# Kernel tuning notes

Hardware: AMD Instinct MI355X
Metric: run time of the kernel (lower is better)

## Reference

```python
import jax, jax.numpy as jnp
import numpy as np

VOCAB = 32000
MAXLEN = 512
E = 768
H = 12
D = E // H  # 64
L = 6
F = int(E * 8 / 3)  # 2048
THETA = 10000.0
EPS = 1.1920929e-07  # torch.finfo(float32).eps, RMSNorm default


def _rms_norm(x, w):
    var = jnp.mean(x * x, axis=-1, keepdims=True)
    return x * jax.lax.rsqrt(var + EPS) * w


def _rope(x, cos, sin):
    # x: [B,H,C,D]; cos/sin: [C,D/2] (interleaved even/odd convention)
    xe = x[..., 0::2]
    xo = x[..., 1::2]
    re = xe * cos - xo * sin
    ro = xe * sin + xo * cos
    out = jnp.stack([re, ro], axis=-1)  # [B,H,C,D/2,2]
    return out.reshape(x.shape)


def setup_inputs() -> dict:
    key = jax.random.key(0)
    ks = jax.random.split(key, 13)
    s = 0.02
    ids = jax.random.randint(ks[0], (8, MAXLEN), 0, VOCAB)
    embed = jax.random.normal(ks[1], (VOCAB, E), jnp.float32) * s
    norm1_w = jnp.ones((L, E), jnp.float32)
    wq = jax.random.normal(ks[2], (L, E, H * D), jnp.float32) * s
    wk = jax.random.normal(ks[3], (L, E, H * D), jnp.float32) * s
    wv = jax.random.normal(ks[4], (L, E, H * D), jnp.float32) * s
    wo = jax.random.normal(ks[5], (L, H * D, E), jnp.float32) * s
    norm2_w = jnp.ones((L, E), jnp.float32)
    w_gate = jax.random.normal(ks[6], (L, E, F), jnp.float32) * s
    w_val = jax.random.normal(ks[7], (L, E, F), jnp.float32) * s
    w_out = jax.random.normal(ks[8], (L, F, E), jnp.float32) * s
    normf_w = jnp.ones((E,), jnp.float32)
    unembed = jax.random.normal(ks[9], (E, VOCAB), jnp.float32) * s
    return {"ids": ids, "embed": embed, "norm1_w": norm1_w, "wq": wq,
            "wk": wk, "wv": wv, "wo": wo, "norm2_w": norm2_w,
            "w_gate": w_gate, "w_val": w_val, "w_out": w_out,
            "normf_w": normf_w, "unembed": unembed}


def reference(ids, embed, norm1_w, wq, wk, wv, wo, norm2_w,
              w_gate, w_val, w_out, normf_w, unembed):
    B, C = ids.shape
    # RoPE caches [C, D/2]
    half_ids = jnp.arange(D // 2, dtype=jnp.float32)
    inv_freq = 1.0 / (THETA ** (2.0 * half_ids / D))
    angles = jnp.arange(C, dtype=jnp.float32)[:, None] * inv_freq[None, :]
    cos, sin = jnp.cos(angles), jnp.sin(angles)
    causal = jnp.tril(jnp.ones((C, C), bool))

    x = embed[ids]  # [B,C,E]
    for l in range(L):
        h = _rms_norm(x, norm1_w[l])
        q = (h @ wq[l]).reshape(B, C, H, D).transpose(0, 2, 1, 3)
        k = (h @ wk[l]).reshape(B, C, H, D).transpose(0, 2, 1, 3)
        v = (h @ wv[l]).reshape(B, C, H, D).transpose(0, 2, 1, 3)
        q = _rope(q, cos, sin)
        k = _rope(k, cos, sin)
        scores = jnp.einsum('bhqd,bhkd->bhqk', q, k) / jnp.sqrt(jnp.float32(D))
        scores = jnp.where(causal, scores, -jnp.inf)
        w = jax.nn.softmax(scores, axis=-1)
        attn = jnp.einsum('bhqk,bhkd->bhqd', w, v)
        attn = attn.transpose(0, 2, 1, 3).reshape(B, C, H * D)
        x = x + attn @ wo[l]
        h2 = _rms_norm(x, norm2_w[l])
        gated = jax.nn.silu(h2 @ w_gate[l]) * (h2 @ w_val[l])
        x = x + gated @ w_out[l]
    x = _rms_norm(x, normf_w)
    return x @ unembed  # [B,C,VOCAB]
```

## Files before the change

kernel.cpp:

```cpp
#include <hip/hip_runtime.h>
#include <hip/hip_bf16.h>
#include <stdint.h>

typedef __hip_bfloat16 bf16;
typedef unsigned short ushort_t;
typedef __attribute__((ext_vector_type(8))) short bf16x8;
typedef __attribute__((ext_vector_type(4))) float f32x4;

#define EPSV 1.1920929e-07f

__device__ __forceinline__ float bfu2f(uint32_t u) {
  union { uint32_t i; float f; } t; t.i = u << 16; return t.f;
}
__device__ __forceinline__ ushort_t f2bfu(float f) {
  bf16 h = __float2bfloat16(f);
  return *reinterpret_cast<ushort_t*>(&h);
}

#define BAR() __builtin_amdgcn_s_barrier()
#define SCHEDB() __builtin_amdgcn_sched_barrier(0)
#define WAIT_LGKM0() { asm volatile("s_waitcnt lgkmcnt(0)" ::: "memory"); SCHEDB(); }
#define WAIT_VM4() asm volatile("s_waitcnt vmcnt(4)" ::: "memory")
#define WAIT_VM0() asm volatile("s_waitcnt vmcnt(0)" ::: "memory")

__global__ void rope_table_kernel(float* __restrict__ cosT, float* __restrict__ sinT) {
  int i = blockIdx.x * 256 + threadIdx.x;
  if (i >= 512 * 32) return;
  int c = i >> 5, dp = i & 31;
  float inv = powf(10000.0f, -(2.0f * dp) / 64.0f);
  float a = (float)c * inv;
  cosT[i] = cosf(a);
  sinT[i] = sinf(a);
}

__global__ void embed_kernel(const int* __restrict__ ids, const float* __restrict__ emb,
                             float* __restrict__ x) {
  int t = blockIdx.x;
  int id = ids[t];
  const float4* s = (const float4*)(emb + (size_t)id * 768);
  float4* d = (float4*)(x + (size_t)t * 768);
  d[threadIdx.x] = s[threadIdx.x];
}

__global__ __launch_bounds__(256) void rmsnorm_kernel(const float* __restrict__ x,
                                                      const float* __restrict__ wgt,
                                                      bf16* __restrict__ out) {
  const int row = blockIdx.x;
  const int tid = threadIdx.x;
  const float* xr = x + (size_t)row * 768;
  float v0 = xr[tid], v1 = xr[tid + 256], v2 = xr[tid + 512];
  float s = v0 * v0 + v1 * v1 + v2 * v2;
#pragma unroll
  for (int d = 1; d < 64; d <<= 1) s += __shfl_xor(s, d);
  __shared__ float red[4];
  if ((tid & 63) == 0) red[tid >> 6] = s;
  __syncthreads();
  s = red[0] + red[1] + red[2] + red[3];
  float rs = rsqrtf(s * (1.0f / 768.0f) + EPSV);
  bf16* orow = out + (size_t)row * 768;
  orow[tid]       = __float2bfloat16(v0 * rs * wgt[tid]);
  orow[tid + 256] = __float2bfloat16(v1 * rs * wgt[tid + 256]);
  orow[tid + 512] = __float2bfloat16(v2 * rs * wgt[tid + 512]);
}

__global__ __launch_bounds__(256) void transpose_all_kernel(
    const float* __restrict__ wq, const float* __restrict__ wk,
    const float* __restrict__ wv, const float* __restrict__ wo,
    const float* __restrict__ wg, const float* __restrict__ wvl,
    const float* __restrict__ wout, const float* __restrict__ unemb,
    bf16* __restrict__ wqkvT, bf16* __restrict__ woT,
    bf16* __restrict__ wgvT, bf16* __restrict__ woutT,
    bf16* __restrict__ unembT) {
  int id = blockIdx.x;
  const float* src; bf16* dst; int K, N, tile;
  bool gvmode = false; int w2 = 0;
  if (id < 13824) {
    int m = id / 576; tile = id % 576;
    int l = m >> 2, w3 = m & 3;
    K = 768; N = 768;
    const float* s0 = (w3 == 0) ? wq : (w3 == 1) ? wk : (w3 == 2) ? wv : wo;
    src = s0 + (size_t)l * 768 * 768;
    dst = (w3 < 3) ? wqkvT + (size_t)l * 2304 * 768 + (size_t)w3 * 768 * 768
                   : woT + (size_t)l * 768 * 768;
  } else if (id < 32256) {
    int id2 = id - 13824; int m = id2 / 1536; tile = id2 % 1536;
    int l = m >> 1; w2 = m & 1;
    K = 768; N = 2048; gvmode = true;
    src = (w2 ? wvl : wg) + (size_t)l * 768 * 2048;
    dst = wgvT + (size_t)l * 4096 * 768;
  } else if (id < 41472) {
    int id2 = id - 32256; int l = id2 / 1536; tile = id2 % 1536;
    K = 2048; N = 768;
    src = wout + (size_t)l * 2048 * 768;
    dst = woutT + (size_t)l * 768 * 2048;
  } else {
    tile = id - 41472;
    K = 768; N = 32000;
    src = unemb; dst = unembT;
  }
  int ntn = N >> 5;
  int nt = (tile % ntn) << 5, kt = (tile / ntn) << 5;
  __shared__ float tl[32][33];
  int tx = threadIdx.x & 31, ty = threadIdx.x >> 5;
#pragma unroll
  for (int i = 0; i < 4; ++i)
    tl[ty + i * 8][tx] = src[(size_t)(kt + ty + i * 8) * N + nt + tx];
  __syncthreads();
#pragma unroll
  for (int i = 0; i < 4; ++i) {
    int n = nt + ty + i * 8;
    size_t nrow = gvmode ? (size_t)((n >> 7) * 256 + w2 * 128 + (n & 127)) : (size_t)n;
    dst[nrow * K + kt + tx] = __float2bfloat16(tl[tx][ty + i * 8]);
  }
}

template <int MODE>
__global__ __launch_bounds__(256) void gemm_bt(const bf16* __restrict__ A,
                                               const bf16* __restrict__ BT,
                                               void* __restrict__ C,
                                               int M, int N, int K) {
  __shared__ __align__(16) bf16 As[128 * 32];
  __shared__ __align__(16) bf16 Bs[128 * 32];
  const int tid = threadIdx.x;
  const int lane = tid & 63, w = tid >> 6;
  const int g = lane >> 4, lc = lane & 15;
  const int bm = blockIdx.y * 128, bn = blockIdx.x * 128;
  const int wm = (w >> 1) * 64, wn = (w & 1) * 64;

  f32x4 acc[4][4];
#pragma unroll
  for (int i = 0; i < 4; ++i)
#pragma unroll
    for (int j = 0; j < 4; ++j) acc[i][j] = (f32x4){0.f, 0.f, 0.f, 0.f};

  for (int k0 = 0; k0 < K; k0 += 32) {
    __syncthreads();
#pragma unroll
    for (int j = 0; j < 2; ++j) {
      int c = (w * 2 + j) * 64 + lane;
      int row = c >> 2, part = c & 3;
      const bf16* srcA = A + (size_t)(bm + row) * K + k0 + part * 8;
      const bf16* srcB = BT + (size_t)(bn + row) * K + k0 + part * 8;
      __builtin_amdgcn_global_load_lds((const __attribute__((address_space(1))) void*)srcA,
                                       (__attribute__((address_space(3))) void*)(As + (w * 2 + j) * 512),
                                       16, 0, 0);
      __builtin_amdgcn_global_load_lds((const __attribute__((address_space(1))) void*)srcB,
                                       (__attribute__((address_space(3))) void*)(Bs + (w * 2 + j) * 512),
                                       16, 0, 0);
    }
    __syncthreads();
    bf16x8 af[4], bfr[4];
#pragma unroll
    for (int mi = 0; mi < 4; ++mi)
      af[mi] = *(const bf16x8*)(As + (wm + mi * 16 + lc) * 32 + g * 8);
#pragma unroll
    for (int ni = 0; ni < 4; ++ni)
      bfr[ni] = *(const bf16x8*)(Bs + (wn + ni * 16 + lc) * 32 + g * 8);
#pragma unroll
    for (int mi = 0; mi < 4; ++mi)
#pragma unroll
      for (int ni = 0; ni < 4; ++ni)
        acc[mi][ni] = __builtin_amdgcn_mfma_f32_16x16x32_bf16(af[mi], bfr[ni], acc[mi][ni], 0, 0, 0);
  }

#pragma unroll
  for (int mi = 0; mi < 4; ++mi)
#pragma unroll
    for (int ni = 0; ni < 4; ++ni)
#pragma unroll
      for (int r = 0; r < 4; ++r) {
        size_t row = (size_t)bm + wm + mi * 16 + g * 4 + r;
        size_t col = (size_t)bn + wn + ni * 16 + lc;
        float v = acc[mi][ni][r];
        if (MODE == 0)      ((bf16*)C)[row * N + col] = __float2bfloat16(v);
        else if (MODE == 1) ((float*)C)[row * N + col] = v;
        else                ((float*)C)[row * N + col] += v;
      }
}

template <int MODE>
__global__ __launch_bounds__(512, 2) void gemm256(const bf16* __restrict__ A,
                                                  const bf16* __restrict__ BT,
                                                  void* __restrict__ C,
                                                  int M, int N, int K,
                                                  const float* __restrict__ cosT,
                                                  const float* __restrict__ sinT) {
  __shared__ __align__(16) bf16 lds[2][4][256 * 32];

  const int tid = threadIdx.x;
  const int lane = tid & 63, w = tid >> 6;
  const int wr = w >> 2, wc = w & 3;
  const int g = lane >> 4, lc = lane & 15;

  const int nwg = gridDim.x;
  const int q = nwg >> 3;
  const int wg = ((int)blockIdx.x & 7) * q + ((int)blockIdx.x >> 3);
  const int nby = M >> 8;
  const int bx = wg / nby, by = wg % nby;
  const int bm = by << 8, bn = bx << 8;

  const bf16* Ap = A + (size_t)bm * K;
  const bf16* Bp = BT + (size_t)bn * K;

  const int soff = (lc * 64) + ((((lane >> 4) ^ ((lane >> 1) & 3)) << 4));

  auto stage_half = [&](int buf, int slab, const bf16* Base, int kcol) {
#pragma unroll
    for (int j = 0; j < 2; ++j) {
      int half_id = w * 2 + j;
      int row = half_id * 16 + (lane >> 2);
      int s_log = (lane & 3) ^ ((lane >> 3) & 3);
      const bf16* src = Base + (size_t)row * K + kcol + s_log * 8;
      bf16* dst = &lds[buf][slab][half_id * 512];
      __builtin_amdgcn_global_load_lds((const __attribute__((address_space(1))) void*)src,
                                       (__attribute__((address_space(3))) void*)dst,
                                       16, 0, 0);
    }
  };

  f32x4 acc[8][4];
#pragma unroll
  for (int i = 0; i < 8; ++i)
#pragma unroll
    for (int j = 0; j < 4; ++j) acc[i][j] = (f32x4){0.f, 0.f, 0.f, 0.f};

  const int NT = K >> 6;

  stage_half(0, 0, Ap, 0);
  stage_half(0, 1, Bp, 0);
  stage_half(0, 2, Ap, 32);
  stage_half(0, 3, Bp, 32);

  bf16x8 aF[4], bF[4];

  auto ds_A = [&](int buf, int kk, int mh) {
#pragma unroll
    for (int i = 0; i < 4; ++i) {
      int byte = (wr * 128 + mh * 64 + i * 16) * 64 + soff;
      aF[i] = *(const bf16x8*)((const char*)&lds[buf][kk * 2][0] + byte);
    }
  };
  auto ds_B = [&](int buf, int kk) {
#pragma unroll
    for (int nf = 0; nf < 4; ++nf) {
      int rb = (MODE == 3) ? ((nf < 2) ? (wc * 32 + nf * 16) : (128 + wc * 32 + (nf - 2) * 16))
                           : (wc * 64 + nf * 16);
      int byte = rb * 64 + soff;
      bF[nf] = *(const bf16x8*)((const char*)&lds[buf][kk * 2 + 1][0] + byte);
    }
  };
  auto mfma16 = [&](int mh) {
    __builtin_amdgcn_s_setprio(1);
#pragma unroll
    for (int i = 0; i < 4; ++i)
#pragma unroll
      for (int nf = 0; nf < 4; ++nf)
        acc[mh * 4 + i][nf] =
            __builtin_amdgcn_mfma_f32_16x16x32_bf16(aF[i], bF[nf], acc[mh * 4 + i][nf], 0, 0, 0);
    __builtin_amdgcn_s_setprio(0);
  };

  for (int t = 0; t < NT; ++t) {
    const int buf = t & 1;
    const bool pf = (t + 1) < NT;
    const int knext = (t + 1) << 6;

    WAIT_VM4();
    BAR(); SCHEDB();
    if (pf) stage_half(buf ^ 1, 0, Ap, knext);
    ds_A(buf, 0, 0);
    ds_B(buf, 0);
    BAR();
    WAIT_LGKM0();
    mfma16(0);

    if (pf) stage_half(buf ^ 1, 1, Bp, knext);
    ds_A(buf, 0, 1);
    BAR();
    WAIT_LGKM0();
    mfma16(1);

    if (pf) { WAIT_VM4(); } else { WAIT_VM0(); }
    BAR(); SCHEDB();
    if (pf) stage_half(buf ^ 1, 2, Ap, knext + 32);
    ds_A(buf, 1, 0);
    ds_B(buf, 1);
    BAR();
    WAIT_LGKM0();
    mfma16(0);

    if (pf) stage_half(buf ^ 1, 3, Bp, knext + 32);
    ds_A(buf, 1, 1);
    BAR();
    WAIT_LGKM0();
    mfma16(1);
  }

  if (MODE == 3) {
    bf16* act = (bf16*)C;
#pragma unroll
    for (int mf = 0; mf < 8; ++mf)
#pragma unroll
      for (int nf = 0; nf < 2; ++nf)
#pragma unroll
        for (int r = 0; r < 4; ++r) {
          size_t row = (size_t)bm + wr * 128 + mf * 16 + g * 4 + r;
          size_t col = (size_t)(bn >> 1) + wc * 32 + nf * 16 + lc;
          float gg = acc[mf][nf][r];
          float vv = acc[mf][nf + 2][r];
          float sg = gg / (1.0f + __expf(-gg));
          act[row * 2048 + col] = __float2bfloat16(sg * vv);
        }
  } else if (MODE == 4) {
#pragma unroll
    for (int mf = 0; mf < 8; ++mf)
#pragma unroll
      for (int nf = 0; nf < 4; ++nf)
#pragma unroll
        for (int r = 0; r < 4; ++r) {
          int row = bm + wr * 128 + mf * 16 + g * 4 + r;
          int col = bn + wc * 64 + nf * 16 + lc;
          float v = acc[mf][nf][r];
          float p = __shfl_xor(v, 1);
          float outv = v;
          if (col < 1536) {
            int cpos = row & 511;
            int dp = (col & 63) >> 1;
            float cs = cosT[cpos * 32 + dp], sn = sinT[cpos * 32 + dp];
            float o = (col & 1) ? (p * sn + v * cs) : (v * cs - p * sn);
            outv = (col < 768) ? o * 0.125f : o;
          }
          ((bf16*)C)[(size_t)row * N + col] = __float2bfloat16(outv);
        }
  } else {
#pragma unroll
    for (int mf = 0; mf < 8; ++mf)
#pragma unroll
      for (int nf = 0; nf < 4; ++nf)
#pragma unroll
        for (int r = 0; r < 4; ++r) {
          size_t row = (size_t)bm + wr * 128 + mf * 16 + g * 4 + r;
          size_t col = (size_t)bn + wc * 64 + nf * 16 + lc;
          float v = acc[mf][nf][r];
          if (MODE == 0) ((bf16*)C)[row * N + col] = __float2bfloat16(v);
          else           ((float*)C)[row * N + col] = v;
        }
  }
}

__global__ __launch_bounds__(256) void attn_kernel(const bf16* __restrict__ qkv,
                                                   bf16* __restrict__ out) {
  const int qt = blockIdx.x;
  const int h  = blockIdx.y;
  const int b  = blockIdx.z;
  const int tid = threadIdx.x;
  const int lane = tid & 63, w = tid >> 6;
  const int g = lane >> 4, lc = lane & 15;

  __shared__ __align__(16) bf16 Ks[64 * 64];
  __shared__ __align__(16) bf16 Vt[64][72];
  __shared__ __align__(16) bf16 Pl[4][32][72];

  bf16x8 qa[2][2];
#pragma unroll
  for (int mi = 0; mi < 2; ++mi)
#pragma unroll
    for (int ks = 0; ks < 2; ++ks) {
      size_t t = (size_t)b * 512 + qt * 128 + w * 32 + mi * 16 + lc;
      qa[mi][ks] = *(const bf16x8*)(qkv + t * 2304 + h * 64 + ks * 32 + g * 8);
    }

  float m_r[2][4], l_r[2][4];
  f32x4 acc_o[2][4];
#pragma unroll
  for (int mi = 0; mi < 2; ++mi)
#pragma unroll
    for (int r = 0; r < 4; ++r) { m_r[mi][r] = -1e30f; l_r[mi][r] = 0.f; }
#pragma unroll
  for (int mi = 0; mi < 2; ++mi)
#pragma unroll
    for (int ni = 0; ni < 4; ++ni) acc_o[mi][ni] = (f32x4){0.f, 0.f, 0.f, 0.f};

  const int nkt = 2 * qt + 2;
  for (int kt = 0; kt < nkt; ++kt) {
    __syncthreads();
#pragma unroll
    for (int j = 0; j < 2; ++j) {
      int c = j * 256 + tid;
      int r = c >> 3;
      int s_log = (c & 7) ^ (r & 7);
      const bf16* src = qkv + ((size_t)b * 512 + kt * 64 + r) * 2304 + 768 + h * 64 + s_log * 8;
      bf16* dst = Ks + (j * 2048 + w * 512);
      __builtin_amdgcn_global_load_lds((const __attribute__((address_space(1))) void*)src,
                                       (__attribute__((address_space(3))) void*)dst,
                                       16, 0, 0);
    }
#pragma unroll
    for (int j = 0; j < 2; ++j) {
      int u = j * 256 + tid;
      int r = u >> 3, d0 = (u & 7) * 8;
      bf16x8 vv = *(const bf16x8*)(qkv + ((size_t)b * 512 + kt * 64 + r) * 2304 + 1536 + h * 64 + d0);
#pragma unroll
      for (int e = 0; e < 8; ++e)
        *(ushort_t*)&Vt[d0 + e][r] = (ushort_t)vv[e];
    }
    __syncthreads();

    f32x4 sacc[2][4];
#pragma unroll
    for (int mi = 0; mi < 2; ++mi)
#pragma unroll
      for (int ni = 0; ni < 4; ++ni) sacc[mi][ni] = (f32x4){0.f, 0.f, 0.f, 0.f};
#pragma unroll
    for (int ni = 0; ni < 4; ++ni) {
      int kr = ni * 16 + lc;
      const char* kb = (const char*)Ks + kr * 128;
      bf16x8 kb0 = *(const bf16x8*)(kb + ((g) ^ (kr & 7)) * 16);
      bf16x8 kb1 = *(const bf16x8*)(kb + ((4 + g) ^ (kr & 7)) * 16);
#pragma unroll
      for (int mi = 0; mi < 2; ++mi) {
        sacc[mi][ni] = __builtin_amdgcn_mfma_f32_16x16x32_bf16(qa[mi][0], kb0, sacc[mi][ni], 0, 0, 0);
        sacc[mi][ni] = __builtin_amdgcn_mfma_f32_16x16x32_bf16(qa[mi][1], kb1, sacc[mi][ni], 0, 0, 0);
      }
    }
    if (kt >= 2 * qt) {
#pragma unroll
      for (int mi = 0; mi < 2; ++mi)
#pragma unroll
        for (int ni = 0; ni < 4; ++ni)
#pragma unroll
          for (int r = 0; r < 4; ++r) {
            int ql = w * 32 + mi * 16 + g * 4 + r;
            int kl = ni * 16 + lc;
            if (kt * 64 + kl > qt * 128 + ql) sacc[mi][ni][r] = -1e30f;
          }
    }
#pragma unroll
    for (int mi = 0; mi < 2; ++mi) {
      float mx[4], sm[4], mn[4], sc[4];
#pragma unroll
      for (int r = 0; r < 4; ++r)
        mx[r] = fmaxf(fmaxf(sacc[mi][0][r], sacc[mi][1][r]), fmaxf(sacc[mi][2][r], sacc[mi][3][r]));
#pragma unroll
      for (int d = 1; d < 16; d <<= 1)
#pragma unroll
        for (int r = 0; r < 4; ++r) mx[r] = fmaxf(mx[r], __shfl_xor(mx[r], d));
#pragma unroll
      for (int r = 0; r < 4; ++r) {
        mn[r] = fmaxf(m_r[mi][r], mx[r]);
        sc[r] = __expf(m_r[mi][r] - mn[r]);
        sm[r] = 0.f;
      }
#pragma unroll
      for (int ni = 0; ni < 4; ++ni)
#pragma unroll
        for (int r = 0; r < 4; ++r) {
          float p = __expf(sacc[mi][ni][r] - mn[r]);
          sacc[mi][ni][r] = p;
          sm[r] += p;
        }
#pragma unroll
      for (int d = 1; d < 16; d <<= 1)
#pragma unroll
        for (int r = 0; r < 4; ++r) sm[r] += __shfl_xor(sm[r], d);
#pragma unroll
      for (int r = 0; r < 4; ++r) {
        l_r[mi][r] = l_r[mi][r] * sc[r] + sm[r];
        m_r[mi][r] = mn[r];
      }
#pragma unroll
      for (int ni = 0; ni < 4; ++ni)
#pragma unroll
        for (int r = 0; r < 4; ++r) acc_o[mi][ni][r] *= sc[r];
#pragma unroll
      for (int ni = 0; ni < 4; ++ni)
#pragma unroll
        for (int r = 0; r < 4; ++r)
          *(ushort_t*)&Pl[w][mi * 16 + g * 4 + r][ni * 16 + lc] = f2bfu(sacc[mi][ni][r]);
    }
    WAIT_LGKM0();
#pragma unroll
    for (int ks = 0; ks < 2; ++ks) {
      bf16x8 pa[2];
#pragma unroll
      for (int mi = 0; mi < 2; ++mi)
        pa[mi] = *(const bf16x8*)&Pl[w][mi * 16 + lc][ks * 32 + g * 8];
#pragma unroll
      for (int ni = 0; ni < 4; ++ni) {
        bf16x8 vb = *(const bf16x8*)&Vt[ni * 16 + lc][ks * 32 + g * 8];
#pragma unroll
        for (int mi = 0; mi < 2; ++mi)
          acc_o[mi][ni] = __builtin_amdgcn_mfma_f32_16x16x32_bf16(pa[mi], vb, acc_o[mi][ni], 0, 0, 0);
      }
    }
  }
#pragma unroll
  for (int mi = 0; mi < 2; ++mi) {
    float inv[4];
#pragma unroll
    for (int r = 0; r < 4; ++r) inv[r] = 1.0f / l_r[mi][r];
#pragma unroll
    for (int ni = 0; ni < 4; ++ni)
#pragma unroll
      for (int r = 0; r < 4; ++r) {
        size_t t = (size_t)b * 512 + qt * 128 + w * 32 + mi * 16 + g * 4 + r;
        int d = ni * 16 + lc;
        out[t * 768 + h * 64 + d] = __float2bfloat16(acc_o[mi][ni][r] * inv[r]);
      }
  }
}

extern "C" void kernel_launch(void* const* d_in, const int* in_sizes, int n_in,
                              void* d_out, int out_size, void* d_ws, size_t ws_size,
                              hipStream_t stream) {
  const int*   ids    = (const int*)d_in[0];
  const float* embedW = (const float*)d_in[1];
  const float* norm1w = (const float*)d_in[2];
  const float* wq     = (const float*)d_in[3];
  const float* wk     = (const float*)d_in[4];
  const float* wv     = (const float*)d_in[5];
  const float* wo     = (const float*)d_in[6];
  const float* norm2w = (const float*)d_in[7];
  const float* wgate  = (const float*)d_in[8];
  const float* wval   = (const float*)d_in[9];
  const float* wout   = (const float*)d_in[10];
  const float* normfw = (const float*)d_in[11];
  const float* unemb  = (const float*)d_in[12];

  char* arena = (char*)d_out;
  size_t off = 0;
  auto alloc = [&](size_t bytes) -> char* {
    char* p = arena + off;
    off += (bytes + 255) & ~(size_t)255;
    return p;
  };
  float* x       = (float*)alloc(4096ull * 768 * 4);
  bf16*  h       = (bf16*)alloc(4096ull * 768 * 2);
  bf16*  qkv     = (bf16*)alloc(4096ull * 2304 * 2);
  bf16*  attnout = (bf16*)alloc(4096ull * 768 * 2);
  bf16*  act     = (bf16*)alloc(4096ull * 2048 * 2);
  float* cosT    = (float*)alloc(512 * 32 * 4);
  float* sinT    = (float*)alloc(512 * 32 * 4);
  bf16*  wqkvT   = (bf16*)alloc(6ull * 2304 * 768 * 2);
  bf16*  woT     = (bf16*)alloc(6ull * 768 * 768 * 2);
  bf16*  wgvT    = (bf16*)alloc(6ull * 4096 * 768 * 2);
  bf16*  woutT   = (bf16*)alloc(6ull * 768 * 2048 * 2);

  bf16* unembT = (bf16*)d_ws;
  bf16* hf     = (bf16*)((char*)d_ws + 32000ull * 768 * 2);

  rope_table_kernel<<<64, 256, 0, stream>>>(cosT, sinT);
  embed_kernel<<<4096, 192, 0, stream>>>(ids, embedW, x);
  transpose_all_kernel<<<65472, 256, 0, stream>>>(wq, wk, wv, wo, wgate, wval, wout, unemb,
                                                  wqkvT, woT, wgvT, woutT, unembT);

  for (int l = 0; l < 6; ++l) {
    rmsnorm_kernel<<<4096, 256, 0, stream>>>(x, norm1w + (size_t)l * 768, h);
    gemm256<4><<<16 * 9, 512, 0, stream>>>(h, wqkvT + (size_t)l * 2304 * 768, qkv,
                                           4096, 2304, 768, cosT, sinT);
    attn_kernel<<<dim3(4, 12, 8), 256, 0, stream>>>(qkv, attnout);
    gemm_bt<2><<<dim3(6, 32), 256, 0, stream>>>(attnout, woT + (size_t)l * 768 * 768, x, 4096, 768, 768);
    rmsnorm_kernel<<<4096, 256, 0, stream>>>(x, norm2w + (size_t)l * 768, h);
    gemm256<3><<<16 * 16, 512, 0, stream>>>(h, wgvT + (size_t)l * 4096 * 768, act,
                                            4096, 4096, 768, nullptr, nullptr);
    gemm_bt<2><<<dim3(6, 32), 256, 0, stream>>>(act, woutT + (size_t)l * 768 * 2048, x, 4096, 768, 2048);
  }

  rmsnorm_kernel<<<4096, 256, 0, stream>>>(x, normfw, hf);
  gemm256<1><<<16 * 125, 512, 0, stream>>>(hf, unembT, (float*)d_out, 4096, 32000, 768,
                                           nullptr, nullptr);
}
```

Before: 1.736 ms.

## Split-K the projection GEMMs and fuse residual reduction with RMSNorm

The wo and w_out GEMMs, which previously launched only 192 blocks and did read-modify-write on x, now use split-K (2 and 4 slices) and write partial sums to a new fp32 buffer. A new reduce kernel adds the partials to the residual and computes the next RMSNorm in the same pass, and the embedding gather is fused with the first RMSNorm. The attention kernel's K/V staging also changes from async swizzled LDS loads to plain 32-bit loads into a padded array, with a block barrier in place of the lgkm wait. The aim is better CU occupancy for the narrow GEMMs and fewer launches, at the cost of extra partial-sum memory traffic.

```diff
diff --git a/kernel.cpp b/kernel.cpp
--- a/kernel.cpp
+++ b/kernel.cpp
@@ -33,22 +33,15 @@
   sinT[i] = sinf(a);
 }
 
-__global__ void embed_kernel(const int* __restrict__ ids, const float* __restrict__ emb,
-                             float* __restrict__ x) {
-  int t = blockIdx.x;
-  int id = ids[t];
-  const float4* s = (const float4*)(emb + (size_t)id * 768);
-  float4* d = (float4*)(x + (size_t)t * 768);
-  d[threadIdx.x] = s[threadIdx.x];
-}
-
-__global__ __launch_bounds__(256) void rmsnorm_kernel(const float* __restrict__ x,
-                                                      const float* __restrict__ wgt,
-                                                      bf16* __restrict__ out) {
+__global__ __launch_bounds__(256) void embed_rms_kernel(const int* __restrict__ ids,
+                                                        const float* __restrict__ emb,
+                                                        const float* __restrict__ wgt,
+                                                        float* __restrict__ x,
+                                                        bf16* __restrict__ h) {
   const int row = blockIdx.x;
   const int tid = threadIdx.x;
-  const float* xr = x + (size_t)row * 768;
-  float v0 = xr[tid], v1 = xr[tid + 256], v2 = xr[tid + 512];
+  const float* er = emb + (size_t)ids[row] * 768;
+  float v0 = er[tid], v1 = er[tid + 256], v2 = er[tid + 512];
   float s = v0 * v0 + v1 * v1 + v2 * v2;
 #pragma unroll
   for (int d = 1; d < 64; d <<= 1) s += __shfl_xor(s, d);
@@ -57,10 +50,47 @@
   __syncthreads();
   s = red[0] + red[1] + red[2] + red[3];
   float rs = rsqrtf(s * (1.0f / 768.0f) + EPSV);
-  bf16* orow = out + (size_t)row * 768;
-  orow[tid]       = __float2bfloat16(v0 * rs * wgt[tid]);
-  orow[tid + 256] = __float2bfloat16(v1 * rs * wgt[tid + 256]);
-  orow[tid + 512] = __float2bfloat16(v2 * rs * wgt[tid + 512]);
+  float* xr = x + (size_t)row * 768;
+  bf16* hr = h + (size_t)row * 768;
+  xr[tid] = v0; xr[tid + 256] = v1; xr[tid + 512] = v2;
+  hr[tid]       = __float2bfloat16(v0 * rs * wgt[tid]);
+  hr[tid + 256] = __float2bfloat16(v1 * rs * wgt[tid + 256]);
+  hr[tid + 512] = __float2bfloat16(v2 * rs * wgt[tid + 512]);
+}
+
+template <int S>
+__global__ __launch_bounds__(256) void reduce_rms_kernel(float* __restrict__ x,
+                                                         const float* __restrict__ P,
+                                                         const float* __restrict__ wgt,
+                                                         bf16* __restrict__ h) {
+  const int row = blockIdx.x;
+  const int tid = threadIdx.x;
+  float* xr = x + (size_t)row * 768;
+  float v[3];
+#pragma unroll
+  for (int j = 0; j < 3; ++j) {
+    int c = tid + j * 256;
+    float acc = xr[c];
+#pragma unroll
+    for (int s = 0; s < S; ++s)
+      acc += P[(size_t)s * 4096 * 768 + (size_t)row * 768 + c];
+    v[j] = acc;
+  }
+  float s = v[0] * v[0] + v[1] * v[1] + v[2] * v[2];
+#pragma unroll
+  for (int d = 1; d < 64; d <<= 1) s += __shfl_xor(s, d);
+  __shared__ float red[4];
+  if ((tid & 63) == 0) red[tid >> 6] = s;
+  __syncthreads();
+  s = red[0] + red[1] + red[2] + red[3];
+  float rs = rsqrtf(s * (1.0f / 768.0f) + EPSV);
+  bf16* hr = h + (size_t)row * 768;
+#pragma unroll
+  for (int j = 0; j < 3; ++j) {
+    int c = tid + j * 256;
+    xr[c] = v[j];
+    hr[c] = __float2bfloat16(v[j] * rs * wgt[c]);
+  }
 }
 
 __global__ __launch_bounds__(256) void transpose_all_kernel(
@@ -114,17 +144,18 @@
   }
 }
 
-template <int MODE>
-__global__ __launch_bounds__(256) void gemm_bt(const bf16* __restrict__ A,
-                                               const bf16* __restrict__ BT,
-                                               void* __restrict__ C,
-                                               int M, int N, int K) {
+__global__ __launch_bounds__(256) void gemm_bt_sk(const bf16* __restrict__ A,
+                                                  const bf16* __restrict__ BT,
+                                                  float* __restrict__ P,
+                                                  int M, int N, int KS, int K) {
   __shared__ __align__(16) bf16 As[128 * 32];
   __shared__ __align__(16) bf16 Bs[128 * 32];
   const int tid = threadIdx.x;
   const int lane = tid & 63, w = tid >> 6;
   const int g = lane >> 4, lc = lane & 15;
   const int bm = blockIdx.y * 128, bn = blockIdx.x * 128;
+  const int z = blockIdx.z;
+  const int koff = z * KS;
   const int wm = (w >> 1) * 64, wn = (w & 1) * 64;
 
   f32x4 acc[4][4];
@@ -133,7 +164,7 @@
 #pragma unroll
     for (int j = 0; j < 4; ++j) acc[i][j] = (f32x4){0.f, 0.f, 0.f, 0.f};
 
-  for (int k0 = 0; k0 < K; k0 += 32) {
+  for (int k0 = koff; k0 < koff + KS; k0 += 32) {
     __syncthreads();
 #pragma unroll
     for (int j = 0; j < 2; ++j) {
@@ -163,6 +194,7 @@
         acc[mi][ni] = __builtin_amdgcn_mfma_f32_16x16x32_bf16(af[mi], bfr[ni], acc[mi][ni], 0, 0, 0);
   }
 
+  float* Pz = P + (size_t)z * M * N;
 #pragma unroll
   for (int mi = 0; mi < 4; ++mi)
 #pragma unroll
@@ -171,10 +203,7 @@
       for (int r = 0; r < 4; ++r) {
         size_t row = (size_t)bm + wm + mi * 16 + g * 4 + r;
         size_t col = (size_t)bn + wn + ni * 16 + lc;
-        float v = acc[mi][ni][r];
-        if (MODE == 0)      ((bf16*)C)[row * N + col] = __float2bfloat16(v);
-        else if (MODE == 1) ((float*)C)[row * N + col] = v;
-        else                ((float*)C)[row * N + col] += v;
+        Pz[row * N + col] = acc[mi][ni][r];
       }
 }
 
@@ -357,7 +386,7 @@
   const int lane = tid & 63, w = tid >> 6;
   const int g = lane >> 4, lc = lane & 15;
 
-  __shared__ __align__(16) bf16 Ks[64 * 64];
+  __shared__ __align__(16) bf16 Ks[64][72];
   __shared__ __align__(16) bf16 Vt[64][72];
   __shared__ __align__(16) bf16 Pl[4][32][72];
 
@@ -384,25 +413,15 @@
   const int nkt = 2 * qt + 2;
   for (int kt = 0; kt < nkt; ++kt) {
     __syncthreads();
-#pragma unroll
-    for (int j = 0; j < 2; ++j) {
-      int c = j * 256 + tid;
-      int r = c >> 3;
-      int s_log = (c & 7) ^ (r & 7);
-      const bf16* src = qkv + ((size_t)b * 512 + kt * 64 + r) * 2304 + 768 + h * 64 + s_log * 8;
-      bf16* dst = Ks + (j * 2048 + w * 512);
-      __builtin_amdgcn_global_load_lds((const __attribute__((address_space(1))) void*)src,
-                                       (__attribute__((address_space(3))) void*)dst,
-                                       16, 0, 0);
-    }
-#pragma unroll
-    for (int j = 0; j < 2; ++j) {
-      int u = j * 256 + tid;
-      int r = u >> 3, d0 = (u & 7) * 8;
-      bf16x8 vv = *(const bf16x8*)(qkv + ((size_t)b * 512 + kt * 64 + r) * 2304 + 1536 + h * 64 + d0);
-#pragma unroll
-      for (int e = 0; e < 8; ++e)
-        *(ushort_t*)&Vt[d0 + e][r] = (ushort_t)vv[e];
+    for (int i = 0; i < 8; ++i) {
+      int pi = i * 256 + tid;
+      int r = pi >> 5, dp = pi & 31;
+      size_t t = (size_t)b * 512 + kt * 64 + r;
+      uint32_t u = *(const uint32_t*)(qkv + t * 2304 + 768 + h * 64 + dp * 2);
+      *(uint32_t*)&Ks[r][dp * 2] = u;
+      uint32_t uv = *(const uint32_t*)(qkv + t * 2304 + 1536 + h * 64 + dp * 2);
+      *(ushort_t*)&Vt[dp * 2][r]     = (ushort_t)(uv & 0xffffu);
+      *(ushort_t*)&Vt[dp * 2 + 1][r] = (ushort_t)(uv >> 16);
     }
     __syncthreads();
 
@@ -413,10 +432,8 @@
       for (int ni = 0; ni < 4; ++ni) sacc[mi][ni] = (f32x4){0.f, 0.f, 0.f, 0.f};
 #pragma unroll
     for (int ni = 0; ni < 4; ++ni) {
-      int kr = ni * 16 + lc;
-      const char* kb = (const char*)Ks + kr * 128;
-      bf16x8 kb0 = *(const bf16x8*)(kb + ((g) ^ (kr & 7)) * 16);
-      bf16x8 kb1 = *(const bf16x8*)(kb + ((4 + g) ^ (kr & 7)) * 16);
+      bf16x8 kb0 = *(const bf16x8*)&Ks[ni * 16 + lc][g * 8];
+      bf16x8 kb1 = *(const bf16x8*)&Ks[ni * 16 + lc][32 + g * 8];
 #pragma unroll
       for (int mi = 0; mi < 2; ++mi) {
         sacc[mi][ni] = __builtin_amdgcn_mfma_f32_16x16x32_bf16(qa[mi][0], kb0, sacc[mi][ni], 0, 0, 0);
@@ -478,7 +495,7 @@
         for (int r = 0; r < 4; ++r)
           *(ushort_t*)&Pl[w][mi * 16 + g * 4 + r][ni * 16 + lc] = f2bfu(sacc[mi][ni][r]);
     }
-    WAIT_LGKM0();
+    __syncthreads();
 #pragma unroll
     for (int ks = 0; ks < 2; ++ks) {
       bf16x8 pa[2];
@@ -539,6 +556,7 @@
   bf16*  qkv     = (bf16*)alloc(4096ull * 2304 * 2);
   bf16*  attnout = (bf16*)alloc(4096ull * 768 * 2);
   bf16*  act     = (bf16*)alloc(4096ull * 2048 * 2);
+  float* part    = (float*)alloc(4ull * 4096 * 768 * 4);
   float* cosT    = (float*)alloc(512 * 32 * 4);
   float* sinT    = (float*)alloc(512 * 32 * 4);
   bf16*  wqkvT   = (bf16*)alloc(6ull * 2304 * 768 * 2);
@@ -550,23 +568,27 @@
   bf16* hf     = (bf16*)((char*)d_ws + 32000ull * 768 * 2);
 
   rope_table_kernel<<<64, 256, 0, stream>>>(cosT, sinT);
-  embed_kernel<<<4096, 192, 0, stream>>>(ids, embedW, x);
   transpose_all_kernel<<<65472, 256, 0, stream>>>(wq, wk, wv, wo, wgate, wval, wout, unemb,
                                                   wqkvT, woT, wgvT, woutT, unembT);
+  embed_rms_kernel<<<4096, 256, 0, stream>>>(ids, embedW, norm1w, x, h);
 
   for (int l = 0; l < 6; ++l) {
-    rmsnorm_kernel<<<4096, 256, 0, stream>>>(x, norm1w + (size_t)l * 768, h);
     gemm256<4><<<16 * 9, 512, 0, stream>>>(h, wqkvT + (size_t)l * 2304 * 768, qkv,
                                            4096, 2304, 768, cosT, sinT);
     attn_kernel<<<dim3(4, 12, 8), 256, 0, stream>>>(qkv, attnout);
-    gemm_bt<2><<<dim3(6, 32), 256, 0, stream>>>(attnout, woT + (size_t)l * 768 * 768, x, 4096, 768, 768);
-    rmsnorm_kernel<<<4096, 256, 0, stream>>>(x, norm2w + (size_t)l * 768, h);
+    gemm_bt_sk<<<dim3(6, 32, 2), 256, 0, stream>>>(attnout, woT + (size_t)l * 768 * 768, part,
+                                                   4096, 768, 384, 768);
+    reduce_rms_kernel<2><<<4096, 256, 0, stream>>>(x, part, norm2w + (size_t)l * 768, h);
     gemm256<3><<<16 * 16, 512, 0, stream>>>(h, wgvT + (size_t)l * 4096 * 768, act,
                                             4096, 4096, 768, nullptr, nullptr);
-    gemm_bt<2><<<dim3(6, 32), 256, 0, stream>>>(act, woutT + (size_t)l * 768 * 2048, x, 4096, 768, 2048);
-  }
-
-  rmsnorm_kernel<<<4096, 256, 0, stream>>>(x, normfw, hf);
+    gemm_bt_sk<<<dim3(6, 32, 4), 256, 0, stream>>>(act, woutT + (size_t)l * 768 * 2048, part,
+                                                   4096, 768, 512, 2048);
+    if (l < 5)
+      reduce_rms_kernel<4><<<4096, 256, 0, stream>>>(x, part, norm1w + (size_t)(l + 1) * 768, h);
+    else
+      reduce_rms_kernel<4><<<4096, 256, 0, stream>>>(x, part, normfw, hf);
+  }
+
   gemm256<1><<<16 * 125, 512, 0, stream>>>(hf, unembT, (float*)d_out, 4096, 32000, 768,
                                            nullptr, nullptr);
 }
```

Result: faster. 1.495 ms (-13.9%).
